# Performance work log

Hardware: AMD Instinct MI355X
Metric: run time of the kernel (lower is better)

## Reference

```python
import jax, jax.numpy as jnp
import numpy as np

B, S, D, H = 2048, 200, 128, 4
H1, H2 = 64, 32
F = 4 * D
TIME_DECAY = 0.1


def setup_inputs() -> dict:
    key = jax.random.key(0)
    ks = jax.random.split(key, 10)
    query = jax.random.normal(ks[0], (B, D), dtype=jnp.float32)
    keys = jax.random.normal(ks[1], (B, S, D), dtype=jnp.float32)
    keys_mask = jax.random.randint(ks[2], (B, S), 0, 2).astype(bool)
    keys_mask = keys_mask.at[:, 0].set(True)  # avoid fully-masked rows
    sc = 0.02
    # per-head MLP params, stacked over heads
    W1 = sc * jax.random.normal(ks[3], (H, H1, F), dtype=jnp.float32)
    b1 = jnp.zeros((H, H1), dtype=jnp.float32)
    a1 = 0.25 * jnp.ones((H,), dtype=jnp.float32)  # PReLU (default single param)
    W2 = sc * jax.random.normal(ks[4], (H, H2, H1), dtype=jnp.float32)
    b2 = jnp.zeros((H, H2), dtype=jnp.float32)
    a2 = 0.25 * jnp.ones((H,), dtype=jnp.float32)
    W3 = sc * jax.random.normal(ks[5], (H, H2), dtype=jnp.float32)
    b3 = jnp.zeros((H,), dtype=jnp.float32)
    Wo = sc * jax.random.normal(ks[6], (D, D), dtype=jnp.float32)
    bo = jnp.zeros((D,), dtype=jnp.float32)
    return {"query": query, "keys": keys, "keys_mask": keys_mask,
            "W1": W1, "b1": b1, "a1": a1, "W2": W2, "b2": b2, "a2": a2,
            "W3": W3, "b3": b3, "Wo": Wo, "bo": bo}


def reference(query, keys, keys_mask, W1, b1, a1, W2, b2, a2, W3, b3, Wo, bo):
    b, s, d = keys.shape
    q = query[:, None, :]                                    # [B,1,D]
    x = jnp.concatenate(
        [keys, jnp.broadcast_to(q, (b, s, d)), keys * q, keys - q], axis=-1)  # [B,S,4D]
    pos = jnp.arange(s, dtype=keys.dtype)
    tw = jnp.exp(TIME_DECAY * (pos - s + 1))                 # [S]
    # all heads batched: [B,H,S,H1]
    h = jnp.einsum('bsf,hdf->bhsd', x, W1) + b1[None, :, None, :]
    h = jnp.where(h >= 0, h, a1[None, :, None, None] * h)    # PReLU
    h = jnp.einsum('bhsd,hed->bhse', h, W2) + b2[None, :, None, :]
    h = jnp.where(h >= 0, h, a2[None, :, None, None] * h)
    scores = jnp.einsum('bhse,he->bhs', h, W3) + b3[None, :, None]
    scores = scores * tw[None, None, :]
    scores = jnp.where(keys_mask[:, None, :], scores, -1e9)
    w = jax.nn.softmax(scores, axis=-1)                      # [B,H,S]
    out_h = jnp.einsum('bhs,bsd->bhd', w, keys)              # [B,H,D]
    combined = out_h.mean(axis=1)                            # [B,D]
    output = combined @ Wo.T + bo                            # [B,D]
    avg_weights = w.mean(axis=1)                             # [B,S]
    return output, avg_weights
```

## Files before the change

kernel.cpp:

```cpp
#include <hip/hip_runtime.h>
#include <hip/hip_bf16.h>
#include <stdint.h>

#define Bsz 2048
#define Ssz 200
#define Dsz 128
#define SP  224

typedef __attribute__((ext_vector_type(8))) short short8;
typedef __attribute__((ext_vector_type(4))) float f32x4;
typedef unsigned short ushort_t;
typedef unsigned int uint_t;

#define LGKM_FENCE() do { asm volatile("s_waitcnt lgkmcnt(0)" ::: "memory"); \
                          __builtin_amdgcn_sched_barrier(0); } while (0)

#define KEYS_OFF   0
#define H1S_OFF    57344
#define SCW_OFF    73728
#define C1S_OFF    77312
#define SMEM_BYTES 78336
#define PO_OFF     57344
#define COMB_OFF   59392
#define PO2_OFF    59904

__device__ __forceinline__ ushort_t cvtbf(float x) {
    union { float f; uint_t u; } v; v.f = x;
    uint_t u = v.u;
    u += 0x7FFFu + ((u >> 16) & 1u);
    return (ushort_t)(u >> 16);
}
__device__ __forceinline__ float bflo(uint_t kv) {
    union { uint_t u; float f; } v; v.u = kv << 16; return v.f;
}
__device__ __forceinline__ float bfhi(uint_t kv) {
    union { uint_t u; float f; } v; v.u = kv & 0xFFFF0000u; return v.f;
}

__global__ void prep_kernel(const float* __restrict__ W1, const float* __restrict__ W2,
                            const float* __restrict__ Wo,
                            float* __restrict__ W1sum, float* __restrict__ W1c,
                            float* __restrict__ W1diffT, float* __restrict__ WoT,
                            ushort_t* __restrict__ W2bf) {
    int i = blockIdx.x * blockDim.x + threadIdx.x;
    if (i < 32768) {
        int n = i >> 7, j = i & 127;
        float a  = W1[n * 512 + j];
        float dd = W1[n * 512 + 384 + j];
        W1sum[i] = a + dd;
        W1c[i]   = W1[n * 512 + 256 + j];
        W1diffT[j * 256 + n] = W1[n * 512 + 128 + j] - dd;
    }
    if (i < 16384) {
        int j = i >> 7, d = i & 127;
        WoT[i] = Wo[d * 128 + j];
    }
    if (i < 8192) W2bf[i] = cvtbf(W2[i]);
}

__launch_bounds__(256, 2)
__global__ void attn_kernel(const float* __restrict__ query, const float* __restrict__ keys,
                            const int* __restrict__ kmask,
                            const float* __restrict__ a1, const float* __restrict__ b2,
                            const float* __restrict__ a2, const float* __restrict__ W3,
                            const float* __restrict__ b3, const float* __restrict__ b1,
                            const float* __restrict__ bo,
                            const float* __restrict__ W1sum, const float* __restrict__ W1c,
                            const float* __restrict__ W1diffT,
                            const float* __restrict__ WoT, const ushort_t* __restrict__ W2bf,
                            float* __restrict__ out) {
    extern __shared__ char smem[];
    const int tid = threadIdx.x;
    const int bb  = blockIdx.x;
    const int w   = tid >> 6;
    const int l   = tid & 63;
    const int l15 = l & 15;
    const int lk  = l >> 4;

    float* scw  = (float*)(smem + SCW_OFF);
    float* c1s  = (float*)(smem + C1S_OFF);
    float* po   = (float*)(smem + PO_OFF);
    float* comb = (float*)(smem + COMB_OFF);
    float* po2  = (float*)(smem + PO2_OFF);
    const float* kb = keys + (size_t)bb * Ssz * Dsz;

    #pragma unroll
    for (int it = 0; it < 28; ++it) {
        int id = tid + 256 * it;
        int row = id >> 5, c4 = id & 31;
        float4 kv = {0.f, 0.f, 0.f, 0.f};
        if (row < Ssz) kv = *(const float4*)(kb + (size_t)row * Dsz + c4 * 4);
        uint_t p0 = (uint_t)cvtbf(kv.x) | ((uint_t)cvtbf(kv.y) << 16);
        uint_t p1 = (uint_t)cvtbf(kv.z) | ((uint_t)cvtbf(kv.w) << 16);
        int off = KEYS_OFF + (((row << 8) + (c4 << 3)) ^ ((row & 7) << 4));
        *(uint_t*)(smem + off)     = p0;
        *(uint_t*)(smem + off + 4) = p1;
    }

    {
        float acc0 = b1[tid], acc1 = 0.f;
        #pragma unroll 4
        for (int j = 0; j < 128; j += 2) {
            acc0 += W1diffT[j * 256 + tid] * query[bb * 128 + j];
            acc1 += W1diffT[(j + 1) * 256 + tid] * query[bb * 128 + j + 1];
        }
        c1s[tid] = acc0 + acc1;
    }

    short8 bfr[16];
    #pragma unroll
    for (int t = 0; t < 4; ++t) {
        const int k0 = t * 32 + lk * 8;
        const float4* pq = (const float4*)(query + bb * 128 + k0);
        float4 q0 = pq[0], q1 = pq[1];
        #pragma unroll
        for (int nt = 0; nt < 4; ++nt) {
            int n = w * 64 + nt * 16 + l15;
            const float4* ps = (const float4*)(W1sum + n * 128 + k0);
            const float4* pc = (const float4*)(W1c + n * 128 + k0);
            float4 s0 = ps[0], s1 = ps[1];
            float4 c0 = pc[0], c1f = pc[1];
            short8 ov;
            ov[0] = (short)cvtbf(s0.x + c0.x * q0.x);
            ov[1] = (short)cvtbf(s0.y + c0.y * q0.y);
            ov[2] = (short)cvtbf(s0.z + c0.z * q0.z);
            ov[3] = (short)cvtbf(s0.w + c0.w * q0.w);
            ov[4] = (short)cvtbf(s1.x + c1f.x * q1.x);
            ov[5] = (short)cvtbf(s1.y + c1f.y * q1.y);
            ov[6] = (short)cvtbf(s1.z + c1f.z * q1.z);
            ov[7] = (short)cvtbf(s1.w + c1f.w * q1.w);
            bfr[t * 4 + nt] = ov;
        }
    }

    const float a1v = a1[w];
    const float a2v = a2[w];
    const float b3v = b3[w];
    float b2v[2], w3v[2];
    #pragma unroll
    for (int nt = 0; nt < 2; ++nt) {
        b2v[nt] = b2[w * 32 + nt * 16 + l15];
        w3v[nt] = W3[w * 32 + nt * 16 + l15];
    }
    short8 w2f[2][2];
    #pragma unroll
    for (int kt = 0; kt < 2; ++kt)
        #pragma unroll
        for (int nt = 0; nt < 2; ++nt)
            w2f[kt][nt] = *(const short8*)(W2bf + w * 2048 + (nt * 16 + l15) * 64 + kt * 32 + lk * 8);

    __syncthreads();

    float c1v[4];
    #pragma unroll
    for (int nt = 0; nt < 4; ++nt) c1v[nt] = c1s[w * 64 + nt * 16 + l15];

    char* h1b = smem + H1S_OFF + w * 4096;
    const f32x4 fz = {0.f, 0.f, 0.f, 0.f};

    #pragma unroll 1
    for (int c = 0; c < 7; ++c) {
        const int TT = (c == 6) ? 1 : 2;
        f32x4 acc[2][4];
        #pragma unroll
        for (int i = 0; i < 2; ++i)
            #pragma unroll
            for (int n = 0; n < 4; ++n) acc[i][n] = fz;

        #pragma unroll
        for (int t = 0; t < 4; ++t) {
            #pragma unroll
            for (int i = 0; i < 2; ++i) {
                if (i < TT) {
                    int row = (c * 2 + i) * 16 + l15;
                    int off = KEYS_OFF + (((row << 8) + (t * 64 + lk * 16)) ^ ((row & 7) << 4));
                    short8 afr = *(const short8*)(smem + off);
                    #pragma unroll
                    for (int nt = 0; nt < 4; ++nt)
                        acc[i][nt] = __builtin_amdgcn_mfma_f32_16x16x32_bf16(afr, bfr[t * 4 + nt], acc[i][nt], 0, 0, 0);
                }
            }
        }

        #pragma unroll
        for (int i = 0; i < 2; ++i) {
            if (i < TT) {
                #pragma unroll
                for (int nt = 0; nt < 4; ++nt) {
                    #pragma unroll
                    for (int r = 0; r < 4; ++r) {
                        float v = acc[i][nt][r] + c1v[nt];
                        v = (v >= 0.f) ? v : a1v * v;
                        int lr = i * 16 + lk * 4 + r;
                        int colb = (nt * 16 + l15) * 2;
                        *(ushort_t*)(h1b + lr * 128 + (colb ^ ((lr & 7) << 4))) = cvtbf(v);
                    }
                }
            }
        }
        LGKM_FENCE();

        #pragma unroll
        for (int t2 = 0; t2 < 2; ++t2) {
            if (t2 < TT) {
                f32x4 acc2[2];
                acc2[0] = fz; acc2[1] = fz;
                #pragma unroll
                for (int kt = 0; kt < 2; ++kt) {
                    int lr = t2 * 16 + l15;
                    short8 afr = *(const short8*)(h1b + lr * 128 + ((kt * 64 + lk * 16) ^ ((lr & 7) << 4)));
                    #pragma unroll
                    for (int nt = 0; nt < 2; ++nt)
                        acc2[nt] = __builtin_amdgcn_mfma_f32_16x16x32_bf16(afr, w2f[kt][nt], acc2[nt], 0, 0, 0);
                }
                #pragma unroll
                for (int r = 0; r < 4; ++r) {
                    float sum = 0.f;
                    #pragma unroll
                    for (int nt = 0; nt < 2; ++nt) {
                        float v = acc2[nt][r] + b2v[nt];
                        v = (v >= 0.f) ? v : a2v * v;
                        sum += v * w3v[nt];
                    }
                    sum += __shfl_xor(sum, 1);
                    sum += __shfl_xor(sum, 2);
                    sum += __shfl_xor(sum, 4);
                    sum += __shfl_xor(sum, 8);
                    if (l15 == 0) {
                        int sg = (c * 2 + t2) * 16 + lk * 4 + r;
                        if (sg < Ssz) {
                            float tw = __expf(0.1f * (float)(sg - (Ssz - 1)));
                            float sc = (sum + b3v) * tw;
                            scw[w * SP + sg] = kmask[bb * Ssz + sg] ? sc : -1.0e9f;
                        }
                    }
                }
            }
        }
        LGKM_FENCE();
    }

    {
        float xv[4], ex[4];
        float mx = -3.0e38f;
        #pragma unroll
        for (int i = 0; i < 4; ++i) {
            int s = l + 64 * i;
            xv[i] = (s < Ssz) ? scw[w * SP + s] : -1.0e30f;
            mx = fmaxf(mx, xv[i]);
        }
        #pragma unroll
        for (int m = 1; m < 64; m <<= 1) mx = fmaxf(mx, __shfl_xor(mx, m));
        float sm = 0.f;
        #pragma unroll
        for (int i = 0; i < 4; ++i) {
            int s = l + 64 * i;
            ex[i] = (s < Ssz) ? __expf(xv[i] - mx) : 0.f;
            sm += ex[i];
        }
        #pragma unroll
        for (int m = 1; m < 64; m <<= 1) sm += __shfl_xor(sm, m);
        float inv = 1.0f / sm;
        #pragma unroll
        for (int i = 0; i < 4; ++i) {
            int s = l + 64 * i;
            if (s < Ssz) scw[w * SP + s] = ex[i] * inv;
        }
    }
    __syncthreads();

    if (tid < Ssz) {
        float aw = 0.25f * (scw[tid] + scw[SP + tid] + scw[2 * SP + tid] + scw[3 * SP + tid]);
        out[Bsz * Dsz + bb * Ssz + tid] = aw;
    }

    {
        float s0 = 0.f, s1 = 0.f;
        #pragma unroll 4
        for (int s = 0; s < Ssz; ++s) {
            float wv = scw[w * SP + s];
            uint_t kv = *(const uint_t*)(smem + KEYS_OFF + (((s << 8) + 4 * l) ^ ((s & 7) << 4)));
            s0 += wv * bflo(kv);
            s1 += wv * bfhi(kv);
        }
        po[w * 128 + 2 * l]     = s0;
        po[w * 128 + 2 * l + 1] = s1;
    }
    __syncthreads();

    if (tid < 128) comb[tid] = 0.25f * (po[tid] + po[128 + tid] + po[256 + tid] + po[384 + tid]);
    __syncthreads();

    {
        int d = tid & 127, part = tid >> 7;
        float o = 0.f;
        const float* wp = WoT + (size_t)part * 64 * 128 + d;
        #pragma unroll 8
        for (int j = 0; j < 64; ++j) o += comb[part * 64 + j] * wp[j * 128];
        po2[part * 128 + d] = o;
    }
    __syncthreads();
    if (tid < 128) out[bb * Dsz + tid] = bo[tid] + po2[tid] + po2[128 + tid];
}

extern "C" void kernel_launch(void* const* d_in, const int* in_sizes, int n_in,
                              void* d_out, int out_size, void* d_ws, size_t ws_size,
                              hipStream_t stream) {
    const float* query = (const float*)d_in[0];
    const float* keys  = (const float*)d_in[1];
    const int*   kmask = (const int*)d_in[2];
    const float* W1    = (const float*)d_in[3];
    const float* b1    = (const float*)d_in[4];
    const float* a1    = (const float*)d_in[5];
    const float* W2    = (const float*)d_in[6];
    const float* b2    = (const float*)d_in[7];
    const float* a2    = (const float*)d_in[8];
    const float* W3    = (const float*)d_in[9];
    const float* b3    = (const float*)d_in[10];
    const float* Wo    = (const float*)d_in[11];
    const float* bo    = (const float*)d_in[12];
    float* out = (float*)d_out;

    char* ws = (char*)d_ws;
    float*    W1sum   = (float*)(ws);
    float*    W1c     = (float*)(ws + 131072);
    float*    W1diffT = (float*)(ws + 262144);
    float*    WoT     = (float*)(ws + 393216);
    ushort_t* W2bf    = (ushort_t*)(ws + 458752);

    hipFuncSetAttribute(reinterpret_cast<const void*>(attn_kernel),
                        hipFuncAttributeMaxDynamicSharedMemorySize, SMEM_BYTES);

    prep_kernel<<<128, 256, 0, stream>>>(W1, W2, Wo, W1sum, W1c, W1diffT, WoT, W2bf);
    attn_kernel<<<Bsz, 256, SMEM_BYTES, stream>>>(query, keys, kmask, a1, b2, a2, W3, b3, b1, bo,
                                                  W1sum, W1c, W1diffT, WoT, W2bf, out);
}
```

Before: 229.0 us.

## Restructure MLP tile loop, use MFMA for weighted key sum, shrink LDS

The MLP score loop now runs over 13 single 16-row tiles with a double-buffered per-wave h1 scratch, replacing the two-tile chunks and their explicit LDS fences. The softmax-weighted key reduction becomes a bf16 MFMA over the stored bf16 weights, where it used to be a scalar loop that summed partials through LDS. Other changes: the keys staging drops the padded rows and uses uint2 stores, c1 is computed from a row-major W1diff with float4 loads, bf16 conversion goes through the library intrinsic, and shared memory shrinks to 72192 bytes. Removing the fences depends on the compiler inserting waits for the LDS write-read dependency within a wave. The MFMA operands are gathered with scalar ushort LDS reads, which may cost more than the MFMA saves.

```diff
diff --git a/kernel.cpp b/kernel.cpp
--- a/kernel.cpp
+++ b/kernel.cpp
@@ -12,35 +12,26 @@
 typedef unsigned short ushort_t;
 typedef unsigned int uint_t;
 
-#define LGKM_FENCE() do { asm volatile("s_waitcnt lgkmcnt(0)" ::: "memory"); \
-                          __builtin_amdgcn_sched_barrier(0); } while (0)
-
 #define KEYS_OFF   0
-#define H1S_OFF    57344
-#define SCW_OFF    73728
-#define C1S_OFF    77312
-#define SMEM_BYTES 78336
-#define PO_OFF     57344
+#define H1S_OFF    51200
+#define SCW_OFF    67584
+#define C1S_OFF    71168
+#define SMEM_BYTES 72192
+#define SCWB_OFF   51200
 #define COMB_OFF   59392
 #define PO2_OFF    59904
 
 __device__ __forceinline__ ushort_t cvtbf(float x) {
-    union { float f; uint_t u; } v; v.f = x;
-    uint_t u = v.u;
-    u += 0x7FFFu + ((u >> 16) & 1u);
-    return (ushort_t)(u >> 16);
-}
-__device__ __forceinline__ float bflo(uint_t kv) {
-    union { uint_t u; float f; } v; v.u = kv << 16; return v.f;
-}
-__device__ __forceinline__ float bfhi(uint_t kv) {
-    union { uint_t u; float f; } v; v.u = kv & 0xFFFF0000u; return v.f;
+    __hip_bfloat16 h = __float2bfloat16(x);
+    ushort_t u;
+    __builtin_memcpy(&u, &h, 2);
+    return u;
 }
 
 __global__ void prep_kernel(const float* __restrict__ W1, const float* __restrict__ W2,
                             const float* __restrict__ Wo,
                             float* __restrict__ W1sum, float* __restrict__ W1c,
-                            float* __restrict__ W1diffT, float* __restrict__ WoT,
+                            float* __restrict__ W1diffR, float* __restrict__ WoT,
                             ushort_t* __restrict__ W2bf) {
     int i = blockIdx.x * blockDim.x + threadIdx.x;
     if (i < 32768) {
@@ -49,7 +40,7 @@
         float dd = W1[n * 512 + 384 + j];
         W1sum[i] = a + dd;
         W1c[i]   = W1[n * 512 + 256 + j];
-        W1diffT[j * 256 + n] = W1[n * 512 + 128 + j] - dd;
+        W1diffR[i] = W1[n * 512 + 128 + j] - dd;
     }
     if (i < 16384) {
         int j = i >> 7, d = i & 127;
@@ -66,7 +57,7 @@
                             const float* __restrict__ b3, const float* __restrict__ b1,
                             const float* __restrict__ bo,
                             const float* __restrict__ W1sum, const float* __restrict__ W1c,
-                            const float* __restrict__ W1diffT,
+                            const float* __restrict__ W1diffR,
                             const float* __restrict__ WoT, const ushort_t* __restrict__ W2bf,
                             float* __restrict__ out) {
     extern __shared__ char smem[];
@@ -79,32 +70,33 @@
 
     float* scw  = (float*)(smem + SCW_OFF);
     float* c1s  = (float*)(smem + C1S_OFF);
-    float* po   = (float*)(smem + PO_OFF);
     float* comb = (float*)(smem + COMB_OFF);
     float* po2  = (float*)(smem + PO2_OFF);
     const float* kb = keys + (size_t)bb * Ssz * Dsz;
 
     #pragma unroll
-    for (int it = 0; it < 28; ++it) {
+    for (int it = 0; it < 25; ++it) {
         int id = tid + 256 * it;
         int row = id >> 5, c4 = id & 31;
-        float4 kv = {0.f, 0.f, 0.f, 0.f};
-        if (row < Ssz) kv = *(const float4*)(kb + (size_t)row * Dsz + c4 * 4);
-        uint_t p0 = (uint_t)cvtbf(kv.x) | ((uint_t)cvtbf(kv.y) << 16);
-        uint_t p1 = (uint_t)cvtbf(kv.z) | ((uint_t)cvtbf(kv.w) << 16);
+        float4 kv = *(const float4*)(kb + (size_t)row * Dsz + c4 * 4);
+        uint2 p;
+        p.x = (uint_t)cvtbf(kv.x) | ((uint_t)cvtbf(kv.y) << 16);
+        p.y = (uint_t)cvtbf(kv.z) | ((uint_t)cvtbf(kv.w) << 16);
         int off = KEYS_OFF + (((row << 8) + (c4 << 3)) ^ ((row & 7) << 4));
-        *(uint_t*)(smem + off)     = p0;
-        *(uint_t*)(smem + off + 4) = p1;
-    }
-
-    {
-        float acc0 = b1[tid], acc1 = 0.f;
-        #pragma unroll 4
-        for (int j = 0; j < 128; j += 2) {
-            acc0 += W1diffT[j * 256 + tid] * query[bb * 128 + j];
-            acc1 += W1diffT[(j + 1) * 256 + tid] * query[bb * 128 + j + 1];
-        }
-        c1s[tid] = acc0 + acc1;
+        *(uint2*)(smem + off) = p;
+    }
+
+    {
+        float accc = b1[tid];
+        const float4* wr  = (const float4*)(W1diffR + tid * 128);
+        const float4* qv4 = (const float4*)(query + bb * 128);
+        #pragma unroll 8
+        for (int j4 = 0; j4 < 32; ++j4) {
+            float4 wv = wr[j4];
+            float4 qq = qv4[j4];
+            accc += wv.x * qq.x + wv.y * qq.y + wv.z * qq.z + wv.w * qq.w;
+        }
+        c1s[tid] = accc;
     }
 
     short8 bfr[16];
@@ -155,93 +147,75 @@
     #pragma unroll
     for (int nt = 0; nt < 4; ++nt) c1v[nt] = c1s[w * 64 + nt * 16 + l15];
 
-    char* h1b = smem + H1S_OFF + w * 4096;
     const f32x4 fz = {0.f, 0.f, 0.f, 0.f};
-
-    #pragma unroll 1
-    for (int c = 0; c < 7; ++c) {
-        const int TT = (c == 6) ? 1 : 2;
-        f32x4 acc[2][4];
-        #pragma unroll
-        for (int i = 0; i < 2; ++i)
-            #pragma unroll
-            for (int n = 0; n < 4; ++n) acc[i][n] = fz;
+    char* h1base = smem + H1S_OFF + w * 4096;
+
+    #pragma unroll 2
+    for (int m = 0; m < 13; ++m) {
+        char* h1b = h1base + (m & 1) * 2048;
+        f32x4 acc[4];
+        #pragma unroll
+        for (int nt = 0; nt < 4; ++nt) acc[nt] = fz;
 
         #pragma unroll
         for (int t = 0; t < 4; ++t) {
-            #pragma unroll
-            for (int i = 0; i < 2; ++i) {
-                if (i < TT) {
-                    int row = (c * 2 + i) * 16 + l15;
-                    int off = KEYS_OFF + (((row << 8) + (t * 64 + lk * 16)) ^ ((row & 7) << 4));
-                    short8 afr = *(const short8*)(smem + off);
-                    #pragma unroll
-                    for (int nt = 0; nt < 4; ++nt)
-                        acc[i][nt] = __builtin_amdgcn_mfma_f32_16x16x32_bf16(afr, bfr[t * 4 + nt], acc[i][nt], 0, 0, 0);
+            int row = m * 16 + l15;
+            row = (row < Ssz) ? row : (Ssz - 1);
+            int off = KEYS_OFF + (((row << 8) + (t * 64 + lk * 16)) ^ ((row & 7) << 4));
+            short8 afr = *(const short8*)(smem + off);
+            #pragma unroll
+            for (int nt = 0; nt < 4; ++nt)
+                acc[nt] = __builtin_amdgcn_mfma_f32_16x16x32_bf16(afr, bfr[t * 4 + nt], acc[nt], 0, 0, 0);
+        }
+
+        #pragma unroll
+        for (int nt = 0; nt < 4; ++nt) {
+            #pragma unroll
+            for (int r = 0; r < 4; ++r) {
+                float v = acc[nt][r] + c1v[nt];
+                v = (v >= 0.f) ? v : a1v * v;
+                int lr = lk * 4 + r;
+                int colb = (nt * 16 + l15) * 2;
+                *(ushort_t*)(h1b + lr * 128 + (colb ^ ((lr & 7) << 4))) = cvtbf(v);
+            }
+        }
+
+        f32x4 acc2[2];
+        acc2[0] = fz; acc2[1] = fz;
+        #pragma unroll
+        for (int kt = 0; kt < 2; ++kt) {
+            short8 afr2 = *(const short8*)(h1b + l15 * 128 + ((kt * 64 + lk * 16) ^ ((l15 & 7) << 4)));
+            #pragma unroll
+            for (int nt = 0; nt < 2; ++nt)
+                acc2[nt] = __builtin_amdgcn_mfma_f32_16x16x32_bf16(afr2, w2f[kt][nt], acc2[nt], 0, 0, 0);
+        }
+        #pragma unroll
+        for (int r = 0; r < 4; ++r) {
+            float sum = 0.f;
+            #pragma unroll
+            for (int nt = 0; nt < 2; ++nt) {
+                float v = acc2[nt][r] + b2v[nt];
+                v = (v >= 0.f) ? v : a2v * v;
+                sum += v * w3v[nt];
+            }
+            sum += __shfl_xor(sum, 1);
+            sum += __shfl_xor(sum, 2);
+            sum += __shfl_xor(sum, 4);
+            sum += __shfl_xor(sum, 8);
+            if (l15 == 0) {
+                int sg = m * 16 + lk * 4 + r;
+                if (sg < Ssz) {
+                    float tw = __expf(0.1f * (float)(sg - (Ssz - 1)));
+                    float sc = (sum + b3v) * tw;
+                    scw[w * SP + sg] = kmask[bb * Ssz + sg] ? sc : -1.0e9f;
                 }
             }
         }
-
-        #pragma unroll
-        for (int i = 0; i < 2; ++i) {
-            if (i < TT) {
-                #pragma unroll
-                for (int nt = 0; nt < 4; ++nt) {
-                    #pragma unroll
-                    for (int r = 0; r < 4; ++r) {
-                        float v = acc[i][nt][r] + c1v[nt];
-                        v = (v >= 0.f) ? v : a1v * v;
-                        int lr = i * 16 + lk * 4 + r;
-                        int colb = (nt * 16 + l15) * 2;
-                        *(ushort_t*)(h1b + lr * 128 + (colb ^ ((lr & 7) << 4))) = cvtbf(v);
-                    }
-                }
-            }
-        }
-        LGKM_FENCE();
-
-        #pragma unroll
-        for (int t2 = 0; t2 < 2; ++t2) {
-            if (t2 < TT) {
-                f32x4 acc2[2];
-                acc2[0] = fz; acc2[1] = fz;
-                #pragma unroll
-                for (int kt = 0; kt < 2; ++kt) {
-                    int lr = t2 * 16 + l15;
-                    short8 afr = *(const short8*)(h1b + lr * 128 + ((kt * 64 + lk * 16) ^ ((lr & 7) << 4)));
-                    #pragma unroll
-                    for (int nt = 0; nt < 2; ++nt)
-                        acc2[nt] = __builtin_amdgcn_mfma_f32_16x16x32_bf16(afr, w2f[kt][nt], acc2[nt], 0, 0, 0);
-                }
-                #pragma unroll
-                for (int r = 0; r < 4; ++r) {
-                    float sum = 0.f;
-                    #pragma unroll
-                    for (int nt = 0; nt < 2; ++nt) {
-                        float v = acc2[nt][r] + b2v[nt];
-                        v = (v >= 0.f) ? v : a2v * v;
-                        sum += v * w3v[nt];
-                    }
-                    sum += __shfl_xor(sum, 1);
-                    sum += __shfl_xor(sum, 2);
-                    sum += __shfl_xor(sum, 4);
-                    sum += __shfl_xor(sum, 8);
-                    if (l15 == 0) {
-                        int sg = (c * 2 + t2) * 16 + lk * 4 + r;
-                        if (sg < Ssz) {
-                            float tw = __expf(0.1f * (float)(sg - (Ssz - 1)));
-                            float sc = (sum + b3v) * tw;
-                            scw[w * SP + sg] = kmask[bb * Ssz + sg] ? sc : -1.0e9f;
-                        }
-                    }
-                }
-            }
-        }
-        LGKM_FENCE();
-    }
-
-    {
-        float xv[4], ex[4];
+    }
+
+    float wv[4];
+    {
+        float xv[4];
         float mx = -3.0e38f;
         #pragma unroll
         for (int i = 0; i < 4; ++i) {
@@ -255,8 +229,8 @@
         #pragma unroll
         for (int i = 0; i < 4; ++i) {
             int s = l + 64 * i;
-            ex[i] = (s < Ssz) ? __expf(xv[i] - mx) : 0.f;
-            sm += ex[i];
+            wv[i] = (s < Ssz) ? __expf(xv[i] - mx) : 0.f;
+            sm += wv[i];
         }
         #pragma unroll
         for (int m = 1; m < 64; m <<= 1) sm += __shfl_xor(sm, m);
@@ -264,8 +238,22 @@
         #pragma unroll
         for (int i = 0; i < 4; ++i) {
             int s = l + 64 * i;
-            if (s < Ssz) scw[w * SP + s] = ex[i] * inv;
-        }
+            wv[i] *= inv;
+            if (s < Ssz) scw[w * SP + s] = wv[i];
+        }
+    }
+    __syncthreads();
+
+    #pragma unroll
+    for (int i = 0; i < 4; ++i) {
+        int s = l + 64 * i;
+        *(ushort_t*)(smem + SCWB_OFF + w * 512 + s * 2) =
+            (s < Ssz) ? cvtbf(wv[i]) : (ushort_t)0;
+    }
+    {
+        uint_t* zb = (uint_t*)(smem + SCWB_OFF + 4 * 512);
+        #pragma unroll
+        for (int k = 0; k < 6; ++k) zb[tid + 256 * k] = 0;
     }
     __syncthreads();
 
@@ -275,20 +263,33 @@
     }
 
     {
-        float s0 = 0.f, s1 = 0.f;
-        #pragma unroll 4
-        for (int s = 0; s < Ssz; ++s) {
-            float wv = scw[w * SP + s];
-            uint_t kv = *(const uint_t*)(smem + KEYS_OFF + (((s << 8) + 4 * l) ^ ((s & 7) << 4)));
-            s0 += wv * bflo(kv);
-            s1 += wv * bfhi(kv);
-        }
-        po[w * 128 + 2 * l]     = s0;
-        po[w * 128 + 2 * l + 1] = s1;
-    }
-    __syncthreads();
-
-    if (tid < 128) comb[tid] = 0.25f * (po[tid] + po[128 + tid] + po[256 + tid] + po[384 + tid]);
+        f32x4 acc4a = fz, acc4b = fz;
+        #pragma unroll
+        for (int t7 = 0; t7 < 7; ++t7) {
+            int kbase = t7 * 32 + lk * 8;
+            short8 afr = *(const short8*)(smem + SCWB_OFF + l15 * 512 + kbase * 2);
+            short8 b2a, b2b;
+            #pragma unroll
+            for (int j = 0; j < 8; ++j) {
+                int s = kbase + j;
+                ushort_t kva = 0, kvb = 0;
+                if (s < Ssz) {
+                    int rowoff = KEYS_OFF + (s << 8);
+                    int sw = (s & 7) << 4;
+                    kva = *(const ushort_t*)(smem + (rowoff + ((32 * w + l15) << 1) ^ sw));
+                    kvb = *(const ushort_t*)(smem + (rowoff + ((32 * w + 16 + l15) << 1) ^ sw));
+                }
+                b2a[j] = (short)kva;
+                b2b[j] = (short)kvb;
+            }
+            acc4a = __builtin_amdgcn_mfma_f32_16x16x32_bf16(afr, b2a, acc4a, 0, 0, 0);
+            acc4b = __builtin_amdgcn_mfma_f32_16x16x32_bf16(afr, b2b, acc4b, 0, 0, 0);
+        }
+        if (lk == 0) {
+            comb[32 * w + l15]      = 0.25f * (acc4a[0] + acc4a[1] + acc4a[2] + acc4a[3]);
+            comb[32 * w + 16 + l15] = 0.25f * (acc4b[0] + acc4b[1] + acc4b[2] + acc4b[3]);
+        }
+    }
     __syncthreads();
 
     {
@@ -324,14 +325,14 @@
     char* ws = (char*)d_ws;
     float*    W1sum   = (float*)(ws);
     float*    W1c     = (float*)(ws + 131072);
-    float*    W1diffT = (float*)(ws + 262144);
+    float*    W1diffR = (float*)(ws + 262144);
     float*    WoT     = (float*)(ws + 393216);
     ushort_t* W2bf    = (ushort_t*)(ws + 458752);
 
     hipFuncSetAttribute(reinterpret_cast<const void*>(attn_kernel),
                         hipFuncAttributeMaxDynamicSharedMemorySize, SMEM_BYTES);
 
-    prep_kernel<<<128, 256, 0, stream>>>(W1, W2, Wo, W1sum, W1c, W1diffT, WoT, W2bf);
+    prep_kernel<<<128, 256, 0, stream>>>(W1, W2, Wo, W1sum, W1c, W1diffR, WoT, W2bf);
     attn_kernel<<<Bsz, 256, SMEM_BYTES, stream>>>(query, keys, kmask, a1, b2, a2, W3, b3, b1, bo,
-                                                  W1sum, W1c, W1diffT, WoT, W2bf, out);
+                                                  W1sum, W1c, W1diffR, WoT, W2bf, out);
 }
```

New measurement: 209.7 us. 8.4% less time.
